# Kernel optimization log

Measured on AMD Instinct MI355X. Metric: run time of the kernel, lower is better.

Reference implementation:

```python
import jax, jax.numpy as jnp
import numpy as np

EPS = 1e-6

def ln2d(x, w, b):
    # LayerNorm over channel dim of NCHW, biased variance, eps=1e-6
    mu = x.mean(1, keepdims=True)
    var = ((x - mu) ** 2).mean(1, keepdims=True)
    y = (x - mu) / jnp.sqrt(var + EPS)
    return w[None, :, None, None] * y + b[None, :, None, None]

def conv1x1(x, w, b):
    # 1x1 conv == pointwise channel mix: w is [C_out, C_in]
    return jnp.einsum('nchw,oc->nohw', x, w) + b[None, :, None, None]

def setup_inputs() -> dict:
    key = jax.random.key(0)
    N, C, H, W = 4, 128, 256, 256
    ks = jax.random.split(key, 8)
    inp = {
        'msi': jax.random.normal(ks[0], (N, C, H, W), jnp.float32),
        'pan': jax.random.normal(ks[1], (N, C, H, W), jnp.float32),
        'ln_w_msi': jnp.ones((C,), jnp.float32),
        'ln_b_msi': jnp.zeros((C,), jnp.float32),
        'ln_w_pan': jnp.ones((C,), jnp.float32),
        'ln_b_pan': jnp.zeros((C,), jnp.float32),
        'w_mp1': jax.random.normal(ks[2], (C, C), jnp.float32) * 0.05,
        'b_mp1': jnp.zeros((C,), jnp.float32),
        'w_pp1': jax.random.normal(ks[3], (C, C), jnp.float32) * 0.05,
        'b_pp1': jnp.zeros((C,), jnp.float32),
        'w_mp2': jax.random.normal(ks[4], (C, C), jnp.float32) * 0.05,
        'b_mp2': jnp.zeros((C,), jnp.float32),
        'w_pp2': jax.random.normal(ks[5], (C, C), jnp.float32) * 0.05,
        'b_pp2': jnp.zeros((C,), jnp.float32),
        'beta': jax.random.normal(ks[6], (1, C, 1, 1), jnp.float32) * 0.1,
        'gamma': jax.random.normal(ks[7], (1, C, 1, 1), jnp.float32) * 0.1,
    }
    return inp

def reference(msi, pan, ln_w_msi, ln_b_msi, ln_w_pan, ln_b_pan,
              w_mp1, b_mp1, w_pp1, b_pp1, w_mp2, b_mp2, w_pp2, b_pp2,
              beta, gamma):
    C = msi.shape[1]
    scale = C ** (-0.5)
    nm = ln2d(msi, ln_w_msi, ln_b_msi)          # norm_msi(msi)
    npn = ln2d(pan, ln_w_pan, ln_b_pan)         # norm_pan(pan)
    q_msi = conv1x1(nm, w_mp1, b_mp1)           # msi_proj1(norm_msi)
    q_pan_from_msi = conv1x1(nm, w_pp1, b_pp1)  # pan_proj1(norm_msi) -- quirk in source
    q_pan = conv1x1(npn, w_pp1, b_pp1)          # pan_proj1(norm_pan)
    v_msi = conv1x1(msi, w_mp2, b_mp2)
    v_pan = conv1x1(pan, w_pp2, b_pp2)
    # per-row attention: contract channels, shared row h -> [N,H,W,W]
    attn_mp = jnp.einsum('nchw,nchv->nhwv', q_msi, q_pan) * scale
    attn_pm = jnp.einsum('nchw,nchv->nhwv', q_pan_from_msi, q_msi) * scale
    f_m2p = jnp.einsum('nhwv,nchv->nchw', jax.nn.softmax(attn_mp, axis=-1), v_pan)
    f_p2m = jnp.einsum('nhwv,nchv->nchw', jax.nn.softmax(attn_pm, axis=-1), v_msi)
    return (msi + f_m2p * beta, pan + f_p2m * gamma)
```

## Files before the change

kernel.cpp:

```cpp
#include <hip/hip_runtime.h>
#include <hip/hip_bf16.h>

typedef __attribute__((ext_vector_type(4))) float f32x4;
typedef __attribute__((ext_vector_type(8))) short s16x8;

#define NB 4
#define CHN 128
#define HH 256
#define WW 256
#define HWSZ (HH*WW)
#define TENSOR_ELEMS ((size_t)NB*CHN*HWSZ)
#define SCALE 0.08838834764831845f
#define SC2 0.12751889550584484f

__device__ __forceinline__ unsigned short f2b(float f) {
    unsigned int u = __builtin_bit_cast(unsigned int, f);
    u += 0x7fffu + ((u >> 16) & 1u);
    return (unsigned short)(u >> 16);
}
__device__ __forceinline__ unsigned int pack2(float a, float b) {
    return (unsigned int)f2b(a) | ((unsigned int)f2b(b) << 16);
}
__device__ __forceinline__ float b2f(unsigned int lo16) {
    return __builtin_bit_cast(float, lo16 << 16);
}

__device__ __forceinline__ void stage_w(uint4* bufW4, const float* __restrict__ W, int t) {
    #pragma unroll
    for (int it = 0; it < 4; ++it) {
        int j = it*512 + t;
        int o = j >> 4, ch = j & 15;
        const float4* wp = (const float4*)(W + o*128 + ch*8);
        float4 a = wp[0], b = wp[1];
        uint4 u;
        u.x = pack2(a.x, a.y); u.y = pack2(a.z, a.w);
        u.z = pack2(b.x, b.y); u.w = pack2(b.z, b.w);
        bufW4[o*16 + (ch ^ (o & 7))] = u;
    }
}

__device__ __forceinline__ void gemm_tile(const uint4* bufW4, const uint4* bufB4,
                                          int wave, int lr, int lg, f32x4 acc[8]) {
    s16x8 af[4];
    int arow = wave*16 + lr;
    #pragma unroll
    for (int ks = 0; ks < 4; ++ks)
        af[ks] = __builtin_bit_cast(s16x8, bufW4[arow*16 + ((ks*4+lg) ^ (arow & 7))]);
    #pragma unroll
    for (int nt = 0; nt < 8; ++nt) {
        int brow = nt*16 + lr;
        #pragma unroll
        for (int ks = 0; ks < 4; ++ks) {
            s16x8 bf = __builtin_bit_cast(s16x8, bufB4[brow*16 + ((ks*4+lg) ^ (brow & 7))]);
            acc[nt] = __builtin_amdgcn_mfma_f32_16x16x32_bf16(af[ks], bf, acc[nt], 0, 0, 0);
        }
    }
}

__device__ __forceinline__ void epi_nhwc(unsigned short* __restrict__ out, const float* __restrict__ bias,
                                         int n, int pos0, int wave, int lr, int lg, const f32x4 acc[8]) {
    int cb = wave*16 + lg*4;
    float bs[4];
    #pragma unroll
    for (int r = 0; r < 4; ++r) bs[r] = bias[cb + r];
    #pragma unroll
    for (int nt = 0; nt < 8; ++nt) {
        size_t rowb = ((size_t)n*HWSZ + pos0 + nt*16 + lr)*CHN + cb;
        uint2 u;
        u.x = pack2(acc[nt][0]+bs[0], acc[nt][1]+bs[1]);
        u.y = pack2(acc[nt][2]+bs[2], acc[nt][3]+bs[3]);
        *(uint2*)(out + rowb) = u;
    }
}

__global__ __launch_bounds__(512)
void proj_kernel(const float* __restrict__ msi, const float* __restrict__ pan,
                 const float* __restrict__ lnw_m, const float* __restrict__ lnb_m,
                 const float* __restrict__ lnw_p, const float* __restrict__ lnb_p,
                 const float* __restrict__ w_mp1, const float* __restrict__ b_mp1,
                 const float* __restrict__ w_pp1, const float* __restrict__ b_pp1,
                 const float* __restrict__ w_mp2, const float* __restrict__ b_mp2,
                 const float* __restrict__ w_pp2, const float* __restrict__ b_pp2,
                 unsigned short* __restrict__ ws_u)
{
    __shared__ uint4 pool[4096];
    __shared__ float red[1024];
    __shared__ float s_mu[128];
    __shared__ float s_rs[128];

    uint4* bufB4 = pool;
    uint4* bufW4 = pool + 2048;
    unsigned short* vbounce = (unsigned short*)pool;

    const int t = threadIdx.x;
    const int isPan = blockIdx.y;
    const int gid = blockIdx.x;
    const int n = gid >> 9;
    const int pos0 = (gid & 511) << 7;

    const int pos = t & 127;
    const int cg = t >> 7;

    const float* src = isPan ? pan : msi;
    const float* lnw = isPan ? lnw_p : lnw_m;
    const float* lnb = isPan ? lnb_p : lnb_m;

    unsigned short* q_msi_t = ws_u;
    unsigned short* q_pfm_t = ws_u + TENSOR_ELEMS;
    unsigned short* q_pan_t = ws_u + 2*TENSOR_ELEMS;
    unsigned short* v_msi   = ws_u + 3*TENSOR_ELEMS;
    unsigned short* v_pan   = ws_u + 4*TENSOR_ELEMS;

    float vals[32];
    {
        const float* p = src + ((size_t)(n*CHN + cg*32))*HWSZ + pos0 + pos;
        #pragma unroll
        for (int j = 0; j < 32; ++j) vals[j] = p[(size_t)j*HWSZ];
    }
    #pragma unroll
    for (int k8 = 0; k8 < 4; ++k8) {
        uint4 u;
        u.x = pack2(vals[k8*8+0], vals[k8*8+1]);
        u.y = pack2(vals[k8*8+2], vals[k8*8+3]);
        u.z = pack2(vals[k8*8+4], vals[k8*8+5]);
        u.w = pack2(vals[k8*8+6], vals[k8*8+7]);
        int chunk = cg*4 + k8;
        bufB4[pos*16 + (chunk ^ (pos & 7))] = u;
    }
    stage_w(bufW4, isPan ? w_pp2 : w_mp2, t);
    __syncthreads();

    const int wave = t >> 6, lane = t & 63, lr = lane & 15, lg = lane >> 4;
    const f32x4 zero4 = {0.f, 0.f, 0.f, 0.f};

    f32x4 acc[8];
    #pragma unroll
    for (int i = 0; i < 8; ++i) acc[i] = zero4;
    gemm_tile(bufW4, bufB4, wave, lr, lg, acc);

    float s = 0.f, q = 0.f;
    #pragma unroll
    for (int j = 0; j < 32; ++j) { s += vals[j]; q += vals[j]*vals[j]; }
    red[t] = s; red[512 + t] = q;
    __syncthreads();

    if (t < 128) {
        float S = red[t] + red[t+128] + red[t+256] + red[t+384];
        float Q = red[512+t] + red[512+t+128] + red[512+t+256] + red[512+t+384];
        float mu = S * (1.0f/128.0f);
        float var = Q * (1.0f/128.0f) - mu*mu;
        s_mu[t] = mu;
        s_rs[t] = rsqrtf(var + 1e-6f);
    }
    {
        const float* bias = isPan ? b_pp2 : b_mp2;
        int cb = wave*16 + lg*4;
        float bs[4];
        #pragma unroll
        for (int r = 0; r < 4; ++r) bs[r] = bias[cb + r];
        #pragma unroll
        for (int nt = 0; nt < 8; ++nt) {
            int p = nt*16 + lr;
            #pragma unroll
            for (int r = 0; r < 4; ++r)
                vbounce[(cb + r)*136 + p] = f2b(acc[nt][r] + bs[r]);
        }
    }
    __syncthreads();

    {
        unsigned short* vout = isPan ? v_pan : v_msi;
        #pragma unroll
        for (int i = 0; i < 4; ++i) {
            int fl = i*512 + t;
            int c = fl >> 4, k = fl & 15;
            uint4 u = *(const uint4*)(vbounce + c*136 + k*8);
            *(uint4*)(vout + ((size_t)(n*CHN + c))*HWSZ + pos0 + k*8) = u;
        }
    }
    {
        float mu = s_mu[pos], rs = s_rs[pos];
        #pragma unroll
        for (int j = 0; j < 32; ++j) {
            int c = cg*32 + j;
            vals[j] = (vals[j] - mu) * rs * lnw[c] + lnb[c];
        }
    }
    __syncthreads();

    #pragma unroll
    for (int k8 = 0; k8 < 4; ++k8) {
        uint4 u;
        u.x = pack2(vals[k8*8+0], vals[k8*8+1]);
        u.y = pack2(vals[k8*8+2], vals[k8*8+3]);
        u.z = pack2(vals[k8*8+4], vals[k8*8+5]);
        u.w = pack2(vals[k8*8+6], vals[k8*8+7]);
        int chunk = cg*4 + k8;
        bufB4[pos*16 + (chunk ^ (pos & 7))] = u;
    }
    stage_w(bufW4, isPan ? w_pp1 : w_mp1, t);
    __syncthreads();

    #pragma unroll
    for (int i = 0; i < 8; ++i) acc[i] = zero4;
    gemm_tile(bufW4, bufB4, wave, lr, lg, acc);
    epi_nhwc(isPan ? q_pan_t : q_msi_t, isPan ? b_pp1 : b_mp1, n, pos0, wave, lr, lg, acc);

    if (!isPan) {
        __syncthreads();
        stage_w(bufW4, w_pp1, t);
        __syncthreads();
        #pragma unroll
        for (int i = 0; i < 8; ++i) acc[i] = zero4;
        gemm_tile(bufW4, bufB4, wave, lr, lg, acc);
        epi_nhwc(q_pfm_t, b_pp1, n, pos0, wave, lr, lg, acc);
    }
}

__global__ __launch_bounds__(512, 2)
void attn_kernel(const unsigned short* __restrict__ ws_u,
                 const float* __restrict__ msi, const float* __restrict__ pan,
                 const float* __restrict__ beta, const float* __restrict__ gamma,
                 float* __restrict__ out)
{
    __shared__ uint4 kp4[4096];
    __shared__ uint4 v4[4096];

    const int t = threadIdx.x;
    const int wave = t >> 6, lane = t & 63, lr = lane & 15, lg = lane >> 4;
    const int bid = blockIdx.x;
    const int path = (bid >> 3) & 1;
    const int nh = (bid >> 4) * 8 + (bid & 7);
    const int n = nh >> 8, h = nh & 255;

    const unsigned short* q_msi_t = ws_u;
    const unsigned short* q_pfm_t = ws_u + TENSOR_ELEMS;
    const unsigned short* q_pan_t = ws_u + 2*TENSOR_ELEMS;
    const unsigned short* v_msi   = ws_u + 3*TENSOR_ELEMS;
    const unsigned short* v_pan   = ws_u + 4*TENSOR_ELEMS;

    const unsigned short* Qp = path ? q_pfm_t : q_msi_t;
    const unsigned short* Kp = path ? q_msi_t : q_pan_t;
    const unsigned short* Vp = path ? v_msi   : v_pan;
    const float* resid = path ? pan : msi;
    const float* mul   = path ? gamma : beta;
    float* outp = out + (path ? TENSOR_ELEMS : (size_t)0);

    const size_t qkBase = (size_t)nh * (256*128);
    const unsigned short* vb = Vp + (size_t)n*CHN*HWSZ + (size_t)h*WW;

    {
        const uint4* g = (const uint4*)(Kp + qkBase);
        #pragma unroll
        for (int it = 0; it < 8; ++it) {
            int i = it*512 + t;
            int v = i >> 4, ch = i & 15;
            kp4[v*16 + (ch ^ (v & 7))] = g[i];
        }
    }
    s16x8 qf0[4], qf1[4];
    {
        int w = wave*16 + lr;
        const uint4* g0 = (const uint4*)(Qp + qkBase + (size_t)w*128);
        const uint4* g1 = (const uint4*)(Qp + qkBase + (size_t)(w + 128)*128);
        #pragma unroll
        for (int ks = 0; ks < 4; ++ks) {
            qf0[ks] = __builtin_bit_cast(s16x8, g0[ks*4 + lg]);
            qf1[ks] = __builtin_bit_cast(s16x8, g1[ks*4 + lg]);
        }
    }
    __syncthreads();

    const f32x4 zero4 = {0.f, 0.f, 0.f, 0.f};
    f32x4 sAcc[16];

    #pragma unroll
    for (int i = 0; i < 16; ++i) sAcc[i] = zero4;
    #pragma unroll
    for (int nt = 0; nt < 16; ++nt) {
        int vrow = nt*16 + lr;
        #pragma unroll
        for (int ks = 0; ks < 4; ++ks) {
            s16x8 kf = __builtin_bit_cast(s16x8, kp4[vrow*16 + ((ks*4+lg) ^ (vrow & 7))]);
            sAcc[nt] = __builtin_amdgcn_mfma_f32_16x16x32_bf16(kf, qf0[ks], sAcc[nt], 0, 0, 0);
        }
    }

    {
        #pragma unroll
        for (int it = 0; it < 8; ++it) {
            int i = it*512 + t;
            int c = i >> 5, ch = i & 31;
            const uint4* g = (const uint4*)(vb + (size_t)c*HWSZ + ch*8);
            v4[c*32 + (ch ^ (c & 7))] = g[0];
        }
    }

    float inv0;
    uint2 pk0[16];
    {
        float mx = -1e30f;
        #pragma unroll
        for (int nt = 0; nt < 16; ++nt) {
            #pragma unroll
            for (int r = 0; r < 4; ++r) mx = fmaxf(mx, sAcc[nt][r]);
        }
        mx = fmaxf(mx, __shfl_xor(mx, 16, 64));
        mx = fmaxf(mx, __shfl_xor(mx, 32, 64));
        float sm = 0.f;
        #pragma unroll
        for (int nt = 0; nt < 16; ++nt) {
            #pragma unroll
            for (int r = 0; r < 4; ++r) {
                float p = exp2f((sAcc[nt][r] - mx) * SC2);
                sAcc[nt][r] = p;
                sm += p;
            }
        }
        sm += __shfl_xor(sm, 16, 64);
        sm += __shfl_xor(sm, 32, 64);
        inv0 = 1.0f / sm;
        #pragma unroll
        for (int nt = 0; nt < 16; ++nt) {
            pk0[nt].x = pack2(sAcc[nt][0], sAcc[nt][1]);
            pk0[nt].y = pack2(sAcc[nt][2], sAcc[nt][3]);
        }
    }

    #pragma unroll
    for (int i = 0; i < 16; ++i) sAcc[i] = zero4;
    #pragma unroll
    for (int nt = 0; nt < 16; ++nt) {
        int vrow = nt*16 + lr;
        #pragma unroll
        for (int ks = 0; ks < 4; ++ks) {
            s16x8 kf = __builtin_bit_cast(s16x8, kp4[vrow*16 + ((ks*4+lg) ^ (vrow & 7))]);
            sAcc[nt] = __builtin_amdgcn_mfma_f32_16x16x32_bf16(kf, qf1[ks], sAcc[nt], 0, 0, 0);
        }
    }
    float inv1;
    uint2 pk1[16];
    {
        float mx = -1e30f;
        #pragma unroll
        for (int nt = 0; nt < 16; ++nt) {
            #pragma unroll
            for (int r = 0; r < 4; ++r) mx = fmaxf(mx, sAcc[nt][r]);
        }
        mx = fmaxf(mx, __shfl_xor(mx, 16, 64));
        mx = fmaxf(mx, __shfl_xor(mx, 32, 64));
        float sm = 0.f;
        #pragma unroll
        for (int nt = 0; nt < 16; ++nt) {
            #pragma unroll
            for (int r = 0; r < 4; ++r) {
                float p = exp2f((sAcc[nt][r] - mx) * SC2);
                sAcc[nt][r] = p;
                sm += p;
            }
        }
        sm += __shfl_xor(sm, 16, 64);
        sm += __shfl_xor(sm, 32, 64);
        inv1 = 1.0f / sm;
        #pragma unroll
        for (int nt = 0; nt < 16; ++nt) {
            pk1[nt].x = pack2(sAcc[nt][0], sAcc[nt][1]);
            pk1[nt].y = pack2(sAcc[nt][2], sAcc[nt][3]);
        }
    }

    __syncthreads();

    unsigned short* pbuf = (unsigned short*)kp4;
    const int wloc = wave*16 + lr;
    const int pb_base = wloc*256 + lg*4;
    const int sw = (lr & 7) << 3;
    const int wrow = wave*16 + lr;

    #pragma unroll
    for (int nt = 0; nt < 16; ++nt)
        *(uint2*)(pbuf + ((pb_base + nt*16) ^ sw)) = pk0[nt];
    f32x4 oAcc0[8];
    #pragma unroll
    for (int i = 0; i < 8; ++i) oAcc0[i] = zero4;
    #pragma unroll
    for (int ks = 0; ks < 8; ++ks) {
        s16x8 pb = __builtin_bit_cast(s16x8, kp4[wrow*32 + ((ks*4+lg) ^ (wrow & 7))]);
        #pragma unroll
        for (int mt = 0; mt < 8; ++mt) {
            int crow = mt*16 + lr;
            s16x8 av = __builtin_bit_cast(s16x8, v4[crow*32 + ((ks*4+lg) ^ (crow & 7))]);
            oAcc0[mt] = __builtin_amdgcn_mfma_f32_16x16x32_bf16(av, pb, oAcc0[mt], 0, 0, 0);
        }
    }
    #pragma unroll
    for (int nt = 0; nt < 16; ++nt)
        *(uint2*)(pbuf + ((pb_base + nt*16) ^ sw)) = pk1[nt];
    f32x4 oAcc1[8];
    #pragma unroll
    for (int i = 0; i < 8; ++i) oAcc1[i] = zero4;
    #pragma unroll
    for (int ks = 0; ks < 8; ++ks) {
        s16x8 pb = __builtin_bit_cast(s16x8, kp4[wrow*32 + ((ks*4+lg) ^ (wrow & 7))]);
        #pragma unroll
        for (int mt = 0; mt < 8; ++mt) {
            int crow = mt*16 + lr;
            s16x8 av = __builtin_bit_cast(s16x8, v4[crow*32 + ((ks*4+lg) ^ (crow & 7))]);
            oAcc1[mt] = __builtin_amdgcn_mfma_f32_16x16x32_bf16(av, pb, oAcc1[mt], 0, 0, 0);
        }
    }
    __syncthreads();

    {
        unsigned short* ob0 = (unsigned short*)kp4;
        unsigned short* ob1 = (unsigned short*)v4;
        #pragma unroll
        for (int mt = 0; mt < 8; ++mt) {
            int cb = mt*16 + lg*4;
            #pragma unroll
            for (int r = 0; r < 4; ++r) {
                ob0[(cb + r)*136 + wloc] = f2b(oAcc0[mt][r] * inv0);
                ob1[(cb + r)*136 + wloc] = f2b(oAcc1[mt][r] * inv1);
            }
        }
    }
    __syncthreads();

    {
        const float* rb = resid + (size_t)n*CHN*HWSZ + (size_t)h*WW;
        float* ob = outp + (size_t)n*CHN*HWSZ + (size_t)h*WW;
        #pragma unroll
        for (int half = 0; half < 2; ++half) {
            const unsigned short* obuf = (const unsigned short*)(half ? v4 : kp4);
            int woff = half * 128;
            #pragma unroll
            for (int i = 0; i < 4; ++i) {
                int fl = i*512 + t;
                int c = fl >> 4, k = fl & 15;
                const float* rp = rb + (size_t)c*HWSZ + woff + k*8;
                f32x4 rA = *(const f32x4*)rp;
                f32x4 rB = *(const f32x4*)(rp + 4);
                uint4 u = *(const uint4*)(obuf + c*136 + k*8);
                float mc = mul[c];
                f32x4 o0, o1;
                o0[0] = rA[0] + b2f(u.x & 0xffffu) * mc;
                o0[1] = rA[1] + b2f(u.x >> 16) * mc;
                o0[2] = rA[2] + b2f(u.y & 0xffffu) * mc;
                o0[3] = rA[3] + b2f(u.y >> 16) * mc;
                o1[0] = rB[0] + b2f(u.z & 0xffffu) * mc;
                o1[1] = rB[1] + b2f(u.z >> 16) * mc;
                o1[2] = rB[2] + b2f(u.w & 0xffffu) * mc;
                o1[3] = rB[3] + b2f(u.w >> 16) * mc;
                float* p = ob + (size_t)c*HWSZ + woff + k*8;
                *(f32x4*)p = o0;
                *(f32x4*)(p + 4) = o1;
            }
        }
    }
}

extern "C" void kernel_launch(void* const* d_in, const int* in_sizes, int n_in,
                              void* d_out, int out_size, void* d_ws, size_t ws_size,
                              hipStream_t stream) {
    (void)in_sizes; (void)n_in; (void)out_size; (void)ws_size;
    const float* msi   = (const float*)d_in[0];
    const float* pan   = (const float*)d_in[1];
    const float* lnw_m = (const float*)d_in[2];
    const float* lnb_m = (const float*)d_in[3];
    const float* lnw_p = (const float*)d_in[4];
    const float* lnb_p = (const float*)d_in[5];
    const float* w_mp1 = (const float*)d_in[6];
    const float* b_mp1 = (const float*)d_in[7];
    const float* w_pp1 = (const float*)d_in[8];
    const float* b_pp1 = (const float*)d_in[9];
    const float* w_mp2 = (const float*)d_in[10];
    const float* b_mp2 = (const float*)d_in[11];
    const float* w_pp2 = (const float*)d_in[12];
    const float* b_pp2 = (const float*)d_in[13];
    const float* beta  = (const float*)d_in[14];
    const float* gamma = (const float*)d_in[15];
    unsigned short* ws_u = (unsigned short*)d_ws;
    float* out = (float*)d_out;

    proj_kernel<<<dim3(2048, 2), 512, 0, stream>>>(
        msi, pan, lnw_m, lnb_m, lnw_p, lnb_p,
        w_mp1, b_mp1, w_pp1, b_pp1, w_mp2, b_mp2, w_pp2, b_pp2, ws_u);
    attn_kernel<<<dim3(2048), 512, 0, stream>>>(
        ws_u, msi, pan, beta, gamma, out);
}
```

Before: 406.2 us.

## Fuse projection kernel into attention kernel, recomputing Q/K/V per row in LDS

Removes the separate projection kernel and its five bf16 workspace tensors. Each attention block now computes LayerNorm plus the 1x1 projections for Q, K and V of its own row directly from the fp32 inputs into shared memory, with weights held in registers. It also prefetches the residual rows early into registers. This trades global write/read traffic and a kernel boundary for extra per-block work: every row's projections are recomputed for both paths, and LDS and register pressure rise.

After: 515.6 us. 26.9% more time.

```diff
diff --git a/kernel.cpp b/kernel.cpp
--- a/kernel.cpp
+++ b/kernel.cpp
@@ -10,7 +10,6 @@
 #define WW 256
 #define HWSZ (HH*WW)
 #define TENSOR_ELEMS ((size_t)NB*CHN*HWSZ)
-#define SCALE 0.08838834764831845f
 #define SC2 0.12751889550584484f
 
 __device__ __forceinline__ unsigned short f2b(float f) {
@@ -25,206 +24,135 @@
     return __builtin_bit_cast(float, lo16 << 16);
 }
 
-__device__ __forceinline__ void stage_w(uint4* bufW4, const float* __restrict__ W, int t) {
-    #pragma unroll
-    for (int it = 0; it < 4; ++it) {
-        int j = it*512 + t;
-        int o = j >> 4, ch = j & 15;
-        const float4* wp = (const float4*)(W + o*128 + ch*8);
-        float4 a = wp[0], b = wp[1];
-        uint4 u;
-        u.x = pack2(a.x, a.y); u.y = pack2(a.z, a.w);
-        u.z = pack2(b.x, b.y); u.w = pack2(b.z, b.w);
-        bufW4[o*16 + (ch ^ (o & 7))] = u;
-    }
-}
-
-__device__ __forceinline__ void gemm_tile(const uint4* bufW4, const uint4* bufB4,
-                                          int wave, int lr, int lg, f32x4 acc[8]) {
+template<bool DOLN, bool VLAYOUT>
+__device__ __forceinline__ void proj_rows(
+    const float* __restrict__ src, size_t rowbase,
+    const float* __restrict__ lnw, const float* __restrict__ lnb,
+    const float* __restrict__ W, const float* __restrict__ bias,
+    uint4* bufB4, float* red, float* s_mu, float* s_rs,
+    unsigned short* dst16, int t)
+{
+    const int pos = t & 127, cg = t >> 7;
+    const int wave = t >> 6, lane = t & 63, lr = lane & 15, lg = lane >> 4;
+
     s16x8 af[4];
-    int arow = wave*16 + lr;
-    #pragma unroll
-    for (int ks = 0; ks < 4; ++ks)
-        af[ks] = __builtin_bit_cast(s16x8, bufW4[arow*16 + ((ks*4+lg) ^ (arow & 7))]);
-    #pragma unroll
-    for (int nt = 0; nt < 8; ++nt) {
-        int brow = nt*16 + lr;
+    {
+        int arow = wave*16 + lr;
         #pragma unroll
         for (int ks = 0; ks < 4; ++ks) {
-            s16x8 bf = __builtin_bit_cast(s16x8, bufB4[brow*16 + ((ks*4+lg) ^ (brow & 7))]);
-            acc[nt] = __builtin_amdgcn_mfma_f32_16x16x32_bf16(af[ks], bf, acc[nt], 0, 0, 0);
-        }
-    }
-}
-
-__device__ __forceinline__ void epi_nhwc(unsigned short* __restrict__ out, const float* __restrict__ bias,
-                                         int n, int pos0, int wave, int lr, int lg, const f32x4 acc[8]) {
-    int cb = wave*16 + lg*4;
+            const float4* wp = (const float4*)(W + arow*128 + ks*32 + lg*8);
+            float4 a = wp[0], b = wp[1];
+            uint4 u;
+            u.x = pack2(a.x, a.y); u.y = pack2(a.z, a.w);
+            u.z = pack2(b.x, b.y); u.w = pack2(b.z, b.w);
+            af[ks] = __builtin_bit_cast(s16x8, u);
+        }
+    }
+    const int cb = wave*16 + lg*4;
     float bs[4];
     #pragma unroll
     for (int r = 0; r < 4; ++r) bs[r] = bias[cb + r];
-    #pragma unroll
-    for (int nt = 0; nt < 8; ++nt) {
-        size_t rowb = ((size_t)n*HWSZ + pos0 + nt*16 + lr)*CHN + cb;
-        uint2 u;
-        u.x = pack2(acc[nt][0]+bs[0], acc[nt][1]+bs[1]);
-        u.y = pack2(acc[nt][2]+bs[2], acc[nt][3]+bs[3]);
-        *(uint2*)(out + rowb) = u;
-    }
-}
-
-__global__ __launch_bounds__(512)
-void proj_kernel(const float* __restrict__ msi, const float* __restrict__ pan,
+
+    #pragma unroll
+    for (int half = 0; half < 2; ++half) {
+        float vals[32];
+        {
+            const float* p = src + rowbase + (size_t)(cg*32)*HWSZ + half*128 + pos;
+            #pragma unroll
+            for (int j = 0; j < 32; ++j) vals[j] = p[(size_t)j*HWSZ];
+        }
+        if (DOLN) {
+            float s = 0.f, q = 0.f;
+            #pragma unroll
+            for (int j = 0; j < 32; ++j) { s += vals[j]; q += vals[j]*vals[j]; }
+            red[t] = s; red[512 + t] = q;
+            __syncthreads();
+            if (t < 128) {
+                float S = red[t] + red[t+128] + red[t+256] + red[t+384];
+                float Q = red[512+t] + red[512+t+128] + red[512+t+256] + red[512+t+384];
+                float mu = S * (1.0f/128.0f);
+                float var = Q * (1.0f/128.0f) - mu*mu;
+                s_mu[t] = mu;
+                s_rs[t] = rsqrtf(var + 1e-6f);
+            }
+            __syncthreads();
+            float mu = s_mu[pos], rs = s_rs[pos];
+            #pragma unroll
+            for (int j = 0; j < 32; ++j) {
+                int c = cg*32 + j;
+                vals[j] = (vals[j] - mu) * rs * lnw[c] + lnb[c];
+            }
+        } else {
+            __syncthreads();
+        }
+        #pragma unroll
+        for (int k8 = 0; k8 < 4; ++k8) {
+            uint4 u;
+            u.x = pack2(vals[k8*8+0], vals[k8*8+1]);
+            u.y = pack2(vals[k8*8+2], vals[k8*8+3]);
+            u.z = pack2(vals[k8*8+4], vals[k8*8+5]);
+            u.w = pack2(vals[k8*8+6], vals[k8*8+7]);
+            int chunk = cg*4 + k8;
+            bufB4[pos*16 + (chunk ^ (pos & 7))] = u;
+        }
+        __syncthreads();
+        const f32x4 zero4 = {0.f, 0.f, 0.f, 0.f};
+        f32x4 acc[8];
+        #pragma unroll
+        for (int i = 0; i < 8; ++i) acc[i] = zero4;
+        #pragma unroll
+        for (int nt = 0; nt < 8; ++nt) {
+            int brow = nt*16 + lr;
+            #pragma unroll
+            for (int ks = 0; ks < 4; ++ks) {
+                s16x8 bf = __builtin_bit_cast(s16x8, bufB4[brow*16 + ((ks*4+lg) ^ (brow & 7))]);
+                acc[nt] = __builtin_amdgcn_mfma_f32_16x16x32_bf16(af[ks], bf, acc[nt], 0, 0, 0);
+            }
+        }
+        if (!VLAYOUT) {
+            const int chunk = wave*2 + (lg >> 1);
+            const int coff = (lg & 1) * 4;
+            #pragma unroll
+            for (int nt = 0; nt < 8; ++nt) {
+                int w = half*128 + nt*16 + lr;
+                uint2 u;
+                u.x = pack2(acc[nt][0]+bs[0], acc[nt][1]+bs[1]);
+                u.y = pack2(acc[nt][2]+bs[2], acc[nt][3]+bs[3]);
+                *(uint2*)(dst16 + (size_t)(w*16 + (chunk ^ (w & 7)))*8 + coff) = u;
+            }
+        } else {
+            #pragma unroll
+            for (int nt = 0; nt < 8; ++nt) {
+                int v = half*128 + nt*16 + lr;
+                int vhi = v >> 3, vlo = v & 7;
+                #pragma unroll
+                for (int r = 0; r < 4; ++r) {
+                    int c = cb + r;
+                    dst16[(size_t)(c*32 + (vhi ^ (c & 7)))*8 + vlo] = f2b(acc[nt][r] + bs[r]);
+                }
+            }
+        }
+    }
+}
+
+__global__ __launch_bounds__(512, 2)
+void sscam_fused(const float* __restrict__ msi, const float* __restrict__ pan,
                  const float* __restrict__ lnw_m, const float* __restrict__ lnb_m,
                  const float* __restrict__ lnw_p, const float* __restrict__ lnb_p,
                  const float* __restrict__ w_mp1, const float* __restrict__ b_mp1,
                  const float* __restrict__ w_pp1, const float* __restrict__ b_pp1,
                  const float* __restrict__ w_mp2, const float* __restrict__ b_mp2,
                  const float* __restrict__ w_pp2, const float* __restrict__ b_pp2,
-                 unsigned short* __restrict__ ws_u)
-{
-    __shared__ uint4 pool[4096];
-    __shared__ float red[1024];
-    __shared__ float s_mu[128];
-    __shared__ float s_rs[128];
-
-    uint4* bufB4 = pool;
-    uint4* bufW4 = pool + 2048;
-    unsigned short* vbounce = (unsigned short*)pool;
-
-    const int t = threadIdx.x;
-    const int isPan = blockIdx.y;
-    const int gid = blockIdx.x;
-    const int n = gid >> 9;
-    const int pos0 = (gid & 511) << 7;
-
-    const int pos = t & 127;
-    const int cg = t >> 7;
-
-    const float* src = isPan ? pan : msi;
-    const float* lnw = isPan ? lnw_p : lnw_m;
-    const float* lnb = isPan ? lnb_p : lnb_m;
-
-    unsigned short* q_msi_t = ws_u;
-    unsigned short* q_pfm_t = ws_u + TENSOR_ELEMS;
-    unsigned short* q_pan_t = ws_u + 2*TENSOR_ELEMS;
-    unsigned short* v_msi   = ws_u + 3*TENSOR_ELEMS;
-    unsigned short* v_pan   = ws_u + 4*TENSOR_ELEMS;
-
-    float vals[32];
-    {
-        const float* p = src + ((size_t)(n*CHN + cg*32))*HWSZ + pos0 + pos;
-        #pragma unroll
-        for (int j = 0; j < 32; ++j) vals[j] = p[(size_t)j*HWSZ];
-    }
-    #pragma unroll
-    for (int k8 = 0; k8 < 4; ++k8) {
-        uint4 u;
-        u.x = pack2(vals[k8*8+0], vals[k8*8+1]);
-        u.y = pack2(vals[k8*8+2], vals[k8*8+3]);
-        u.z = pack2(vals[k8*8+4], vals[k8*8+5]);
-        u.w = pack2(vals[k8*8+6], vals[k8*8+7]);
-        int chunk = cg*4 + k8;
-        bufB4[pos*16 + (chunk ^ (pos & 7))] = u;
-    }
-    stage_w(bufW4, isPan ? w_pp2 : w_mp2, t);
-    __syncthreads();
-
-    const int wave = t >> 6, lane = t & 63, lr = lane & 15, lg = lane >> 4;
-    const f32x4 zero4 = {0.f, 0.f, 0.f, 0.f};
-
-    f32x4 acc[8];
-    #pragma unroll
-    for (int i = 0; i < 8; ++i) acc[i] = zero4;
-    gemm_tile(bufW4, bufB4, wave, lr, lg, acc);
-
-    float s = 0.f, q = 0.f;
-    #pragma unroll
-    for (int j = 0; j < 32; ++j) { s += vals[j]; q += vals[j]*vals[j]; }
-    red[t] = s; red[512 + t] = q;
-    __syncthreads();
-
-    if (t < 128) {
-        float S = red[t] + red[t+128] + red[t+256] + red[t+384];
-        float Q = red[512+t] + red[512+t+128] + red[512+t+256] + red[512+t+384];
-        float mu = S * (1.0f/128.0f);
-        float var = Q * (1.0f/128.0f) - mu*mu;
-        s_mu[t] = mu;
-        s_rs[t] = rsqrtf(var + 1e-6f);
-    }
-    {
-        const float* bias = isPan ? b_pp2 : b_mp2;
-        int cb = wave*16 + lg*4;
-        float bs[4];
-        #pragma unroll
-        for (int r = 0; r < 4; ++r) bs[r] = bias[cb + r];
-        #pragma unroll
-        for (int nt = 0; nt < 8; ++nt) {
-            int p = nt*16 + lr;
-            #pragma unroll
-            for (int r = 0; r < 4; ++r)
-                vbounce[(cb + r)*136 + p] = f2b(acc[nt][r] + bs[r]);
-        }
-    }
-    __syncthreads();
-
-    {
-        unsigned short* vout = isPan ? v_pan : v_msi;
-        #pragma unroll
-        for (int i = 0; i < 4; ++i) {
-            int fl = i*512 + t;
-            int c = fl >> 4, k = fl & 15;
-            uint4 u = *(const uint4*)(vbounce + c*136 + k*8);
-            *(uint4*)(vout + ((size_t)(n*CHN + c))*HWSZ + pos0 + k*8) = u;
-        }
-    }
-    {
-        float mu = s_mu[pos], rs = s_rs[pos];
-        #pragma unroll
-        for (int j = 0; j < 32; ++j) {
-            int c = cg*32 + j;
-            vals[j] = (vals[j] - mu) * rs * lnw[c] + lnb[c];
-        }
-    }
-    __syncthreads();
-
-    #pragma unroll
-    for (int k8 = 0; k8 < 4; ++k8) {
-        uint4 u;
-        u.x = pack2(vals[k8*8+0], vals[k8*8+1]);
-        u.y = pack2(vals[k8*8+2], vals[k8*8+3]);
-        u.z = pack2(vals[k8*8+4], vals[k8*8+5]);
-        u.w = pack2(vals[k8*8+6], vals[k8*8+7]);
-        int chunk = cg*4 + k8;
-        bufB4[pos*16 + (chunk ^ (pos & 7))] = u;
-    }
-    stage_w(bufW4, isPan ? w_pp1 : w_mp1, t);
-    __syncthreads();
-
-    #pragma unroll
-    for (int i = 0; i < 8; ++i) acc[i] = zero4;
-    gemm_tile(bufW4, bufB4, wave, lr, lg, acc);
-    epi_nhwc(isPan ? q_pan_t : q_msi_t, isPan ? b_pp1 : b_mp1, n, pos0, wave, lr, lg, acc);
-
-    if (!isPan) {
-        __syncthreads();
-        stage_w(bufW4, w_pp1, t);
-        __syncthreads();
-        #pragma unroll
-        for (int i = 0; i < 8; ++i) acc[i] = zero4;
-        gemm_tile(bufW4, bufB4, wave, lr, lg, acc);
-        epi_nhwc(q_pfm_t, b_pp1, n, pos0, wave, lr, lg, acc);
-    }
-}
-
-__global__ __launch_bounds__(512, 2)
-void attn_kernel(const unsigned short* __restrict__ ws_u,
-                 const float* __restrict__ msi, const float* __restrict__ pan,
                  const float* __restrict__ beta, const float* __restrict__ gamma,
                  float* __restrict__ out)
 {
-    __shared__ uint4 kp4[4096];
-    __shared__ uint4 v4[4096];
+    __shared__ uint4 regA[4096];
+    __shared__ uint4 regC[4096];
+    __shared__ uint4 bufB4[2048];
+
+    float* red  = (float*)regC;
+    float* s_mu = red + 1024;
+    float* s_rs = s_mu + 128;
 
     const int t = threadIdx.x;
     const int wave = t >> 6, lane = t & 63, lr = lane & 15, lg = lane >> 4;
@@ -233,41 +161,52 @@
     const int nh = (bid >> 4) * 8 + (bid & 7);
     const int n = nh >> 8, h = nh & 255;
 
-    const unsigned short* q_msi_t = ws_u;
-    const unsigned short* q_pfm_t = ws_u + TENSOR_ELEMS;
-    const unsigned short* q_pan_t = ws_u + 2*TENSOR_ELEMS;
-    const unsigned short* v_msi   = ws_u + 3*TENSOR_ELEMS;
-    const unsigned short* v_pan   = ws_u + 4*TENSOR_ELEMS;
-
-    const unsigned short* Qp = path ? q_pfm_t : q_msi_t;
-    const unsigned short* Kp = path ? q_msi_t : q_pan_t;
-    const unsigned short* Vp = path ? v_msi   : v_pan;
+    const float* Ksrc = path ? msi : pan;
+    const float* lnwK = path ? lnw_m : lnw_p;
+    const float* lnbK = path ? lnb_m : lnb_p;
+    const float* WQ = path ? w_pp1 : w_mp1;
+    const float* bQ = path ? b_pp1 : b_mp1;
+    const float* WK = path ? w_mp1 : w_pp1;
+    const float* bK = path ? b_mp1 : b_pp1;
+    const float* WV = path ? w_mp2 : w_pp2;
+    const float* bV = path ? b_mp2 : b_pp2;
     const float* resid = path ? pan : msi;
     const float* mul   = path ? gamma : beta;
     float* outp = out + (path ? TENSOR_ELEMS : (size_t)0);
 
-    const size_t qkBase = (size_t)nh * (256*128);
-    const unsigned short* vb = Vp + (size_t)n*CHN*HWSZ + (size_t)h*WW;
-
-    {
-        const uint4* g = (const uint4*)(Kp + qkBase);
-        #pragma unroll
-        for (int it = 0; it < 8; ++it) {
-            int i = it*512 + t;
-            int v = i >> 4, ch = i & 15;
-            kp4[v*16 + (ch ^ (v & 7))] = g[i];
-        }
-    }
+    const size_t rowbase = (size_t)n*CHN*HWSZ + (size_t)h*WW;
+
+    unsigned short* A16 = (unsigned short*)regA;
+    unsigned short* C16 = (unsigned short*)regC;
+
+    proj_rows<true, false>(msi, rowbase, lnw_m, lnb_m, WQ, bQ,
+                           bufB4, red, s_mu, s_rs, A16, t);
+    __syncthreads();
+
     s16x8 qf0[4], qf1[4];
     {
-        int w = wave*16 + lr;
-        const uint4* g0 = (const uint4*)(Qp + qkBase + (size_t)w*128);
-        const uint4* g1 = (const uint4*)(Qp + qkBase + (size_t)(w + 128)*128);
+        int w0 = wave*16 + lr;
         #pragma unroll
         for (int ks = 0; ks < 4; ++ks) {
-            qf0[ks] = __builtin_bit_cast(s16x8, g0[ks*4 + lg]);
-            qf1[ks] = __builtin_bit_cast(s16x8, g1[ks*4 + lg]);
-        }
+            qf0[ks] = __builtin_bit_cast(s16x8, regA[w0*16 + ((ks*4+lg) ^ (w0 & 7))]);
+            qf1[ks] = __builtin_bit_cast(s16x8, regA[(w0+128)*16 + ((ks*4+lg) ^ (w0 & 7))]);
+        }
+    }
+
+    proj_rows<true, false>(Ksrc, rowbase, lnwK, lnbK, WK, bK,
+                           bufB4, red, s_mu, s_rs, A16, t);
+
+    proj_rows<false, true>(path ? msi : pan, rowbase, lnw_m, lnb_m, WV, bV,
+                           bufB4, red, s_mu, s_rs, C16, t);
+
+    f32x4 r0A[4], r0B[4];
+    #pragma unroll
+    for (int i = 0; i < 4; ++i) {
+        int fl = i*512 + t;
+        int c = fl >> 4, k = fl & 15;
+        const float* p = resid + rowbase + (size_t)c*HWSZ + k*8;
+        r0A[i] = *(const f32x4*)p;
+        r0B[i] = *(const f32x4*)(p + 4);
     }
     __syncthreads();
 
@@ -281,21 +220,10 @@
         int vrow = nt*16 + lr;
         #pragma unroll
         for (int ks = 0; ks < 4; ++ks) {
-            s16x8 kf = __builtin_bit_cast(s16x8, kp4[vrow*16 + ((ks*4+lg) ^ (vrow & 7))]);
+            s16x8 kf = __builtin_bit_cast(s16x8, regA[vrow*16 + ((ks*4+lg) ^ (vrow & 7))]);
             sAcc[nt] = __builtin_amdgcn_mfma_f32_16x16x32_bf16(kf, qf0[ks], sAcc[nt], 0, 0, 0);
         }
     }
-
-    {
-        #pragma unroll
-        for (int it = 0; it < 8; ++it) {
-            int i = it*512 + t;
-            int c = i >> 5, ch = i & 31;
-            const uint4* g = (const uint4*)(vb + (size_t)c*HWSZ + ch*8);
-            v4[c*32 + (ch ^ (c & 7))] = g[0];
-        }
-    }
-
     float inv0;
     uint2 pk0[16];
     {
@@ -334,7 +262,7 @@
         int vrow = nt*16 + lr;
         #pragma unroll
         for (int ks = 0; ks < 4; ++ks) {
-            s16x8 kf = __builtin_bit_cast(s16x8, kp4[vrow*16 + ((ks*4+lg) ^ (vrow & 7))]);
+            s16x8 kf = __builtin_bit_cast(s16x8, regA[vrow*16 + ((ks*4+lg) ^ (vrow & 7))]);
             sAcc[nt] = __builtin_amdgcn_mfma_f32_16x16x32_bf16(kf, qf1[ks], sAcc[nt], 0, 0, 0);
         }
     }
@@ -369,9 +297,19 @@
         }
     }
 
+    f32x4 r1A[4], r1B[4];
+    #pragma unroll
+    for (int i = 0; i < 4; ++i) {
+        int fl = i*512 + t;
+        int c = fl >> 4, k = fl & 15;
+        const float* p = resid + rowbase + (size_t)c*HWSZ + 128 + k*8;
+        r1A[i] = *(const f32x4*)p;
+        r1B[i] = *(const f32x4*)(p + 4);
+    }
+
     __syncthreads();
 
-    unsigned short* pbuf = (unsigned short*)kp4;
+    unsigned short* pbuf = (unsigned short*)regA;
     const int wloc = wave*16 + lr;
     const int pb_base = wloc*256 + lg*4;
     const int sw = (lr & 7) << 3;
@@ -385,11 +323,11 @@
     for (int i = 0; i < 8; ++i) oAcc0[i] = zero4;
     #pragma unroll
     for (int ks = 0; ks < 8; ++ks) {
-        s16x8 pb = __builtin_bit_cast(s16x8, kp4[wrow*32 + ((ks*4+lg) ^ (wrow & 7))]);
+        s16x8 pb = __builtin_bit_cast(s16x8, regA[wrow*32 + ((ks*4+lg) ^ (wrow & 7))]);
         #pragma unroll
         for (int mt = 0; mt < 8; ++mt) {
             int crow = mt*16 + lr;
-            s16x8 av = __builtin_bit_cast(s16x8, v4[crow*32 + ((ks*4+lg) ^ (crow & 7))]);
+            s16x8 av = __builtin_bit_cast(s16x8, regC[crow*32 + ((ks*4+lg) ^ (crow & 7))]);
             oAcc0[mt] = __builtin_amdgcn_mfma_f32_16x16x32_bf16(av, pb, oAcc0[mt], 0, 0, 0);
         }
     }
@@ -401,19 +339,19 @@
     for (int i = 0; i < 8; ++i) oAcc1[i] = zero4;
     #pragma unroll
     for (int ks = 0; ks < 8; ++ks) {
-        s16x8 pb = __builtin_bit_cast(s16x8, kp4[wrow*32 + ((ks*4+lg) ^ (wrow & 7))]);
+        s16x8 pb = __builtin_bit_cast(s16x8, regA[wrow*32 + ((ks*4+lg) ^ (wrow & 7))]);
         #pragma unroll
         for (int mt = 0; mt < 8; ++mt) {
             int crow = mt*16 + lr;
-            s16x8 av = __builtin_bit_cast(s16x8, v4[crow*32 + ((ks*4+lg) ^ (crow & 7))]);
+            s16x8 av = __builtin_bit_cast(s16x8, regC[crow*32 + ((ks*4+lg) ^ (crow & 7))]);
             oAcc1[mt] = __builtin_amdgcn_mfma_f32_16x16x32_bf16(av, pb, oAcc1[mt], 0, 0, 0);
         }
     }
     __syncthreads();
 
     {
-        unsigned short* ob0 = (unsigned short*)kp4;
-        unsigned short* ob1 = (unsigned short*)v4;
+        unsigned short* ob0 = (unsigned short*)regA;
+        unsigned short* ob1 = (unsigned short*)regC;
         #pragma unroll
         for (int mt = 0; mt < 8; ++mt) {
             int cb = mt*16 + lg*4;
@@ -427,19 +365,17 @@
     __syncthreads();
 
     {
-        const float* rb = resid + (size_t)n*CHN*HWSZ + (size_t)h*WW;
-        float* ob = outp + (size_t)n*CHN*HWSZ + (size_t)h*WW;
+        float* ob = outp + rowbase;
         #pragma unroll
         for (int half = 0; half < 2; ++half) {
-            const unsigned short* obuf = (const unsigned short*)(half ? v4 : kp4);
+            const unsigned short* obuf = (const unsigned short*)(half ? regC : regA);
             int woff = half * 128;
             #pragma unroll
             for (int i = 0; i < 4; ++i) {
                 int fl = i*512 + t;
                 int c = fl >> 4, k = fl & 15;
-                const float* rp = rb + (size_t)c*HWSZ + woff + k*8;
-                f32x4 rA = *(const f32x4*)rp;
-                f32x4 rB = *(const f32x4*)(rp + 4);
+                f32x4 rA = half ? r1A[i] : r0A[i];
+                f32x4 rB = half ? r1B[i] : r0B[i];
                 uint4 u = *(const uint4*)(obuf + c*136 + k*8);
                 float mc = mul[c];
                 f32x4 o0, o1;
@@ -462,7 +398,7 @@
 extern "C" void kernel_launch(void* const* d_in, const int* in_sizes, int n_in,
                               void* d_out, int out_size, void* d_ws, size_t ws_size,
                               hipStream_t stream) {
-    (void)in_sizes; (void)n_in; (void)out_size; (void)ws_size;
+    (void)in_sizes; (void)n_in; (void)out_size; (void)d_ws; (void)ws_size;
     const float* msi   = (const float*)d_in[0];
     const float* pan   = (const float*)d_in[1];
     const float* lnw_m = (const float*)d_in[2];
@@ -479,12 +415,10 @@
     const float* b_pp2 = (const float*)d_in[13];
     const float* beta  = (const float*)d_in[14];
     const float* gamma = (const float*)d_in[15];
-    unsigned short* ws_u = (unsigned short*)d_ws;
     float* out = (float*)d_out;
 
-    proj_kernel<<<dim3(2048, 2), 512, 0, stream>>>(
+    sscam_fused<<<dim3(2048), 512, 0, stream>>>(
         msi, pan, lnw_m, lnb_m, lnw_p, lnb_p,
-        w_mp1, b_mp1, w_pp1, b_pp1, w_mp2, b_mp2, w_pp2, b_pp2, ws_u);
-    attn_kernel<<<dim3(2048), 512, 0, stream>>>(
-        ws_u, msi, pan, beta, gamma, out);
-}
+        w_mp1, b_mp1, w_pp1, b_pp1, w_mp2, b_mp2, w_pp2, b_pp2,
+        beta, gamma, out);
+}
```
